# Optimization experiments

Measured on AMD Instinct MI355X. Metric: run time of the kernel, lower is better.

The kernel has to match this reference:

```python
import jax, jax.numpy as jnp
import numpy as np

B, T, E, H, O = 64, 512, 512, 512, 512

def setup_inputs() -> dict:
    key = jax.random.key(0)
    k1, k2, k3, k4, k5 = jax.random.split(key, 5)
    s1 = 1.0 / np.sqrt(E + H)
    s2 = 1.0 / np.sqrt(H)
    return {
        "x": jax.random.normal(k1, (B, T, E), dtype=jnp.float32),
        "W1": jax.random.uniform(k2, (H, E + H), dtype=jnp.float32, minval=-s1, maxval=s1),
        "b1": jax.random.uniform(k3, (H,), dtype=jnp.float32, minval=-s1, maxval=s1),
        "W2": jax.random.uniform(k4, (O, H), dtype=jnp.float32, minval=-s2, maxval=s2),
        "b2": jax.random.uniform(k5, (O,), dtype=jnp.float32, minval=-s2, maxval=s2),
    }

def reference(x, W1, b1, W2, b2):
    b = x.shape[0]
    h0 = jnp.zeros((b, x.shape[2]), dtype=x.dtype)

    def step(hidden, xt):
        inp = jnp.concatenate([xt, hidden], axis=1)          # [b, e+h]
        hidden = jax.nn.relu(inp @ W1.T + b1)                # [b, h]
        out = hidden @ W2.T + b2                             # [b, o]
        return hidden, out

    # scan over time: x -> [t, b, e]
    h_final, outs = jax.lax.scan(step, h0, jnp.swapaxes(x, 0, 1))
    return jnp.swapaxes(outs, 0, 1), h_final
```

## Files before the change

### kernel.cpp

```cpp
#include <hip/hip_runtime.h>
#include <cstddef>

#define T_STEPS 512
#define BATCH   64
#define EDIM    512
#define HDIM    512
#define ODIM    512

#define HPAD    520
#define W_ELEMS (32 * 4 * 64 * 8)
#define H_ELEMS (16 * HPAD)
#define SMEM_BYTES ((W_ELEMS + H_ELEMS) * 2)

typedef __bf16 bf16;
typedef __bf16 bf16x4 __attribute__((ext_vector_type(4)));
typedef __bf16 bf16x8 __attribute__((ext_vector_type(8)));
typedef float  f32x4  __attribute__((ext_vector_type(4)));

template <typename XT, bool REMAP>
__global__ __launch_bounds__(256) void gemm_mfma_kernel(
    const XT* __restrict__ X, int ldx,
    const float* __restrict__ W, int ldw, int kw0,
    const float* __restrict__ bias,
    float* __restrict__ C, int ldc, int K)
{
  __shared__ __align__(16) bf16 Asm[8 * 64 * 8];
  __shared__ __align__(16) bf16 Bsm[8 * 64 * 8];

  const int tid  = threadIdx.x;
  const int row0 = blockIdx.x * 128;
  const int col0 = blockIdx.y * 128;
  const int w    = tid >> 6, lane = tid & 63;
  const int q    = lane >> 4, nl = lane & 15;
  const int wm   = w >> 1, wn = w & 1;

  f32x4 acc[4][4] = {};

  for (int k0 = 0; k0 < K; k0 += 32) {
#pragma unroll
    for (int rep = 0; rep < 2; ++rep) {
      int idx = tid + rep * 256;
      int mt = idx >> 6, l2 = idx & 63;
      const XT* src = X + (size_t)(row0 + mt * 16 + (l2 & 15)) * ldx
                        + k0 + (l2 >> 4) * 8;
      bf16x8 v;
#pragma unroll
      for (int u = 0; u < 8; ++u) v[u] = (bf16)(float)src[u];
      *(bf16x8*)&Asm[(size_t)idx * 8] = v;
    }
#pragma unroll
    for (int rep = 0; rep < 2; ++rep) {
      int idx = tid + rep * 256;
      int nt = idx >> 6, l2 = idx & 63;
      const float* src = W + (size_t)(col0 + nt * 16 + (l2 & 15)) * ldw
                           + kw0 + k0 + (l2 >> 4) * 8;
      bf16x8 v;
#pragma unroll
      for (int u = 0; u < 8; ++u) v[u] = (bf16)src[u];
      *(bf16x8*)&Bsm[(size_t)idx * 8] = v;
    }
    __syncthreads();

    bf16x8 a[4], b[4];
#pragma unroll
    for (int i = 0; i < 4; ++i)
      a[i] = *(bf16x8*)&Asm[(size_t)((wm * 4 + i) * 64 + lane) * 8];
#pragma unroll
    for (int j = 0; j < 4; ++j)
      b[j] = *(bf16x8*)&Bsm[(size_t)((wn * 4 + j) * 64 + lane) * 8];
#pragma unroll
    for (int i = 0; i < 4; ++i)
#pragma unroll
      for (int j = 0; j < 4; ++j)
        acc[i][j] = __builtin_amdgcn_mfma_f32_16x16x32_bf16(a[i], b[j], acc[i][j], 0, 0, 0);
    __syncthreads();
  }

#pragma unroll
  for (int i = 0; i < 4; ++i)
#pragma unroll
    for (int j = 0; j < 4; ++j) {
      int colg = col0 + wn * 64 + j * 16 + nl;
#pragma unroll
      for (int r = 0; r < 4; ++r) {
        size_t rowg = (size_t)(row0 + wm * 64 + i * 16 + q * 4 + r);
        size_t crow = REMAP ? (((rowg & (T_STEPS - 1)) << 6) | (rowg >> 9)) : rowg;
        C[crow * ldc + colg] = acc[i][j][r] + bias[colg];
      }
    }
}

__global__ __launch_bounds__(512, 2) void scan_big_kernel(
    const float* __restrict__ A,
    const float* __restrict__ W1,
    bf16* __restrict__ Hbf)
{
  extern __shared__ __align__(16) bf16 smem[];
  bf16* Wlds = smem;
  bf16* hsm  = smem + W_ELEMS;

  const int tid  = threadIdx.x;
  const int c    = blockIdx.x;
  const int w    = tid >> 6, lane = tid & 63;
  const int q    = lane >> 4, nl = lane & 15;
  const int rb0  = c * 16;

  for (int idx = tid; idx < 32 * 4 * 64; idx += 512) {
    int l  = idx & 63;
    int kt = (idx >> 6) & 3;
    int tg = idx >> 8;
    int n  = tg * 16 + (l & 15);
    int k  = kt * 32 + (l >> 4) * 8;
    const float* src = W1 + (size_t)n * (EDIM + HDIM) + EDIM + k;
    bf16x8 v;
#pragma unroll
    for (int u = 0; u < 8; ++u) v[u] = (bf16)src[u];
    *(bf16x8*)&Wlds[(size_t)idx * 8] = v;
  }

  bf16x8 Wreg[4][12];
#pragma unroll
  for (int i = 0; i < 4; ++i) {
    int n = w * 64 + i * 16 + nl;
    const float* wrow = W1 + (size_t)n * (EDIM + HDIM) + EDIM;
#pragma unroll
    for (int kt2 = 0; kt2 < 12; ++kt2) {
      const float* src = wrow + (kt2 + 4) * 32 + q * 8;
      bf16x8 v;
#pragma unroll
      for (int u = 0; u < 8; ++u) v[u] = (bf16)src[u];
      Wreg[i][kt2] = v;
    }
  }
  __syncthreads();

  f32x4 An[4];
  {
    const float* ap = A + (size_t)(rb0 + nl) * HDIM + w * 64 + q * 4;
    An[0] = *(const f32x4*)(ap);
    An[1] = *(const f32x4*)(ap + 16);
    An[2] = *(const f32x4*)(ap + 32);
    An[3] = *(const f32x4*)(ap + 48);
  }

  f32x4  acc[4];
  bf16x4 hprev[4];

  for (int t = 0; t < T_STEPS; ++t) {
    if (t > 0) {
      bf16* dst = Hbf + ((size_t)(rb0 + nl) * T_STEPS + (t - 1)) * HDIM
                  + w * 64 + q * 4;
      *(bf16x4*)(dst)      = hprev[0];
      *(bf16x4*)(dst + 16) = hprev[1];
      *(bf16x4*)(dst + 32) = hprev[2];
      *(bf16x4*)(dst + 48) = hprev[3];
    }

#pragma unroll
    for (int i = 0; i < 4; ++i) acc[i] = An[i];
    {
      int tn = (t + 1 < T_STEPS) ? t + 1 : 0;
      const float* ap = A + ((size_t)tn * BATCH + rb0 + nl) * HDIM + w * 64 + q * 4;
      An[0] = *(const f32x4*)(ap);
      An[1] = *(const f32x4*)(ap + 16);
      An[2] = *(const f32x4*)(ap + 32);
      An[3] = *(const f32x4*)(ap + 48);
    }

    if (t > 0) {
#pragma unroll
      for (int kt = 0; kt < 16; ++kt) {
        bf16x8 af = *(bf16x8*)&hsm[nl * HPAD + kt * 32 + q * 8];
        if (kt < 4) {
#pragma unroll
          for (int i = 0; i < 4; ++i) {
            bf16x8 wb = *(bf16x8*)&Wlds[(size_t)(((w * 4 + i) * 4 + kt) * 64 + lane) * 8];
            acc[i] = __builtin_amdgcn_mfma_f32_16x16x32_bf16(wb, af, acc[i], 0, 0, 0);
          }
        } else {
#pragma unroll
          for (int i = 0; i < 4; ++i)
            acc[i] = __builtin_amdgcn_mfma_f32_16x16x32_bf16(Wreg[i][kt - 4], af, acc[i], 0, 0, 0);
        }
      }
    }

    __syncthreads();

#pragma unroll
    for (int i = 0; i < 4; ++i) {
      bf16x4 hv;
#pragma unroll
      for (int r = 0; r < 4; ++r) {
        float v = acc[i][r] > 0.0f ? acc[i][r] : 0.0f;
        hv[r] = (bf16)v;
      }
      *(bf16x4*)&hsm[nl * HPAD + w * 64 + i * 16 + q * 4] = hv;
      hprev[i] = hv;
    }

    __syncthreads();
  }

  {
    bf16* dst = Hbf + ((size_t)(rb0 + nl) * T_STEPS + (T_STEPS - 1)) * HDIM
                + w * 64 + q * 4;
    *(bf16x4*)(dst)      = hprev[0];
    *(bf16x4*)(dst + 16) = hprev[1];
    *(bf16x4*)(dst + 32) = hprev[2];
    *(bf16x4*)(dst + 48) = hprev[3];
  }
}

__global__ __launch_bounds__(256) void copy_hfinal_kernel(
    const bf16* __restrict__ Hbf, float* __restrict__ out)
{
  int i = blockIdx.x * blockDim.x + threadIdx.x;
  int b = i / HDIM, n = i % HDIM;
  out[i] = (float)Hbf[((size_t)b * T_STEPS + (T_STEPS - 1)) * HDIM + n];
}

extern "C" void kernel_launch(void* const* d_in, const int* in_sizes, int n_in,
                              void* d_out, int out_size, void* d_ws, size_t ws_size,
                              hipStream_t stream) {
  const float* x  = (const float*)d_in[0];
  const float* W1 = (const float*)d_in[1];
  const float* b1 = (const float*)d_in[2];
  const float* W2 = (const float*)d_in[3];
  const float* b2 = (const float*)d_in[4];

  float* out = (float*)d_out;
  float* A   = out;

  bf16* Hbf  = (bf16*)d_ws;

  {
    dim3 grid(BATCH * T_STEPS / 128, HDIM / 128);
    gemm_mfma_kernel<float, true><<<grid, 256, 0, stream>>>(
        x, EDIM, W1, EDIM + HDIM, 0, b1, A, HDIM, EDIM);
  }

  hipFuncSetAttribute(
      reinterpret_cast<const void*>(scan_big_kernel),
      hipFuncAttributeMaxDynamicSharedMemorySize, SMEM_BYTES);
  scan_big_kernel<<<4, 512, SMEM_BYTES, stream>>>(A, W1, Hbf);

  {
    dim3 grid(BATCH * T_STEPS / 128, ODIM / 128);
    gemm_mfma_kernel<bf16, false><<<grid, 256, 0, stream>>>(
        Hbf, HDIM, W2, HDIM, 0, b2, out, ODIM, HDIM);
  }

  copy_hfinal_kernel<<<(BATCH * HDIM) / 256, 256, 0, stream>>>(
      Hbf, out + (size_t)BATCH * T_STEPS * ODIM);
}
```

Baseline: 1.608 ms.

## Double-buffer hidden state in LDS to drop one barrier per scan step

The recurrent scan kernel now ping-pongs the hidden-state tile between two LDS buffers, so only one barrier per timestep is needed instead of two. The barrier becomes an LDS-only wait (lgkmcnt) plus s_barrier. The padded row layout is replaced by an XOR swizzle, and the global store of h is issued in the same step it is produced instead of one step later. This adds LDS usage, and a single-buffer fallback is launched if the larger shared-memory request fails.

New measurement: 1.422 ms. -11.6%, faster.

```diff
diff --git a/kernel.cpp b/kernel.cpp
--- a/kernel.cpp
+++ b/kernel.cpp
@@ -7,15 +7,18 @@
 #define HDIM    512
 #define ODIM    512
 
-#define HPAD    520
-#define W_ELEMS (32 * 4 * 64 * 8)
-#define H_ELEMS (16 * HPAD)
-#define SMEM_BYTES ((W_ELEMS + H_ELEMS) * 2)
+#define W_ELEMS  (32 * 4 * 64 * 8)
+#define HB_ELEMS (16 * 512)
 
 typedef __bf16 bf16;
 typedef __bf16 bf16x4 __attribute__((ext_vector_type(4)));
 typedef __bf16 bf16x8 __attribute__((ext_vector_type(8)));
 typedef float  f32x4  __attribute__((ext_vector_type(4)));
+
+__device__ __forceinline__ void barrier_lds() {
+  asm volatile("s_waitcnt lgkmcnt(0)\n\ts_barrier" ::: "memory");
+  __builtin_amdgcn_sched_barrier(0);
+}
 
 template <typename XT, bool REMAP>
 __global__ __launch_bounds__(256) void gemm_mfma_kernel(
@@ -90,20 +93,24 @@
     }
 }
 
-__global__ __launch_bounds__(512, 2) void scan_big_kernel(
+template <int DBUF>
+__global__ __launch_bounds__(512, 2) void scan_kernel(
     const float* __restrict__ A,
     const float* __restrict__ W1,
     bf16* __restrict__ Hbf)
 {
   extern __shared__ __align__(16) bf16 smem[];
   bf16* Wlds = smem;
-  bf16* hsm  = smem + W_ELEMS;
+  bf16* hb0  = smem + W_ELEMS;
+  bf16* hb1  = DBUF ? (hb0 + HB_ELEMS) : hb0;
 
   const int tid  = threadIdx.x;
   const int c    = blockIdx.x;
   const int w    = tid >> 6, lane = tid & 63;
   const int q    = lane >> 4, nl = lane & 15;
   const int rb0  = c * 16;
+  const int n0   = w * 64;
+  const int sw   = (nl & 7) << 3;
 
   for (int idx = tid; idx < 32 * 4 * 64; idx += 512) {
     int l  = idx & 63;
@@ -121,7 +128,7 @@
   bf16x8 Wreg[4][12];
 #pragma unroll
   for (int i = 0; i < 4; ++i) {
-    int n = w * 64 + i * 16 + nl;
+    int n = n0 + i * 16 + nl;
     const float* wrow = W1 + (size_t)n * (EDIM + HDIM) + EDIM;
 #pragma unroll
     for (int kt2 = 0; kt2 < 12; ++kt2) {
@@ -136,31 +143,24 @@
 
   f32x4 An[4];
   {
-    const float* ap = A + (size_t)(rb0 + nl) * HDIM + w * 64 + q * 4;
+    const float* ap = A + (size_t)(rb0 + nl) * HDIM + n0 + q * 4;
     An[0] = *(const f32x4*)(ap);
     An[1] = *(const f32x4*)(ap + 16);
     An[2] = *(const f32x4*)(ap + 32);
     An[3] = *(const f32x4*)(ap + 48);
   }
 
-  f32x4  acc[4];
-  bf16x4 hprev[4];
+  f32x4 acc[4];
 
   for (int t = 0; t < T_STEPS; ++t) {
-    if (t > 0) {
-      bf16* dst = Hbf + ((size_t)(rb0 + nl) * T_STEPS + (t - 1)) * HDIM
-                  + w * 64 + q * 4;
-      *(bf16x4*)(dst)      = hprev[0];
-      *(bf16x4*)(dst + 16) = hprev[1];
-      *(bf16x4*)(dst + 32) = hprev[2];
-      *(bf16x4*)(dst + 48) = hprev[3];
-    }
+    bf16* hr = (t & 1) ? hb1 : hb0;
+    bf16* hw = (t & 1) ? hb0 : hb1;
 
 #pragma unroll
     for (int i = 0; i < 4; ++i) acc[i] = An[i];
     {
       int tn = (t + 1 < T_STEPS) ? t + 1 : 0;
-      const float* ap = A + ((size_t)tn * BATCH + rb0 + nl) * HDIM + w * 64 + q * 4;
+      const float* ap = A + ((size_t)tn * BATCH + rb0 + nl) * HDIM + n0 + q * 4;
       An[0] = *(const f32x4*)(ap);
       An[1] = *(const f32x4*)(ap + 16);
       An[2] = *(const f32x4*)(ap + 32);
@@ -170,7 +170,7 @@
     if (t > 0) {
 #pragma unroll
       for (int kt = 0; kt < 16; ++kt) {
-        bf16x8 af = *(bf16x8*)&hsm[nl * HPAD + kt * 32 + q * 8];
+        bf16x8 af = *(bf16x8*)&hr[nl * 512 + ((kt * 32 + q * 8) ^ sw)];
         if (kt < 4) {
 #pragma unroll
           for (int i = 0; i < 4; ++i) {
@@ -185,7 +185,7 @@
       }
     }
 
-    __syncthreads();
+    if (!DBUF) barrier_lds();
 
 #pragma unroll
     for (int i = 0; i < 4; ++i) {
@@ -195,20 +195,12 @@
         float v = acc[i][r] > 0.0f ? acc[i][r] : 0.0f;
         hv[r] = (bf16)v;
       }
-      *(bf16x4*)&hsm[nl * HPAD + w * 64 + i * 16 + q * 4] = hv;
-      hprev[i] = hv;
-    }
-
-    __syncthreads();
-  }
-
-  {
-    bf16* dst = Hbf + ((size_t)(rb0 + nl) * T_STEPS + (T_STEPS - 1)) * HDIM
-                + w * 64 + q * 4;
-    *(bf16x4*)(dst)      = hprev[0];
-    *(bf16x4*)(dst + 16) = hprev[1];
-    *(bf16x4*)(dst + 32) = hprev[2];
-    *(bf16x4*)(dst + 48) = hprev[3];
+      *(bf16x4*)&hw[nl * 512 + ((n0 + i * 16 + q * 4) ^ sw)] = hv;
+      *(bf16x4*)(Hbf + ((size_t)(rb0 + nl) * T_STEPS + t) * HDIM
+                 + n0 + i * 16 + q * 4) = hv;
+    }
+
+    barrier_lds();
   }
 }
 
@@ -240,10 +232,21 @@
         x, EDIM, W1, EDIM + HDIM, 0, b1, A, HDIM, EDIM);
   }
 
-  hipFuncSetAttribute(
-      reinterpret_cast<const void*>(scan_big_kernel),
-      hipFuncAttributeMaxDynamicSharedMemorySize, SMEM_BYTES);
-  scan_big_kernel<<<4, 512, SMEM_BYTES, stream>>>(A, W1, Hbf);
+  {
+    int smem_dbuf = (W_ELEMS + 2 * HB_ELEMS) * 2;
+    int smem_sbuf = (W_ELEMS + 1 * HB_ELEMS) * 2;
+    hipError_t e = hipFuncSetAttribute(
+        reinterpret_cast<const void*>(scan_kernel<1>),
+        hipFuncAttributeMaxDynamicSharedMemorySize, smem_dbuf);
+    if (e == hipSuccess) {
+      scan_kernel<1><<<4, 512, smem_dbuf, stream>>>(A, W1, Hbf);
+    } else {
+      hipFuncSetAttribute(
+          reinterpret_cast<const void*>(scan_kernel<0>),
+          hipFuncAttributeMaxDynamicSharedMemorySize, smem_sbuf);
+      scan_kernel<0><<<4, 512, smem_sbuf, stream>>>(A, W1, Hbf);
+    }
+  }
 
   {
     dim3 grid(BATCH * T_STEPS / 128, ODIM / 128);
```
